# Kernel optimization log

Measured on AMD Instinct MI355X. Metric: run time of the kernel, lower is better.

The kernel has to match this reference:

```python
import jax, jax.numpy as jnp
import numpy as np

B, T, D = 4, 8160, 1024
N, H = 8, 128            # heads, units_per_head (D == N*H)
W = 12                   # block_size
LEFT_CTX = 13            # atten_left_context
L = LEFT_CTX - 1         # left context frames beyond current position
R = 0                    # atten_right_context
C = W + L + R            # context_size = 24
CAP = 50.0               # attention_logits_soft_capping


def _timing_signal(pos, channels):
    # sinusoidal embedding, channels even (1024)
    pos = pos.astype(jnp.float32)
    nt = channels // 2
    inc = np.log(10000.0) / max(nt - 1, 1)
    inv = jnp.exp(jnp.arange(nt, dtype=jnp.float32) * -inc)
    st = pos[:, :, None] * inv[None, None, :]
    return jnp.concatenate([jnp.sin(st), jnp.cos(st)], axis=2)


def _extract_block_context(x, block_size, left, right, pad_val):
    # x: [B, T, ...] -> [B, num_blocks, context_size, ...]
    pads = [(0, 0)] * x.ndim
    pads[1] = (left, right + block_size - 1)
    xp = jnp.pad(x, pads, constant_values=jnp.asarray(pad_val, x.dtype))
    frame_len = block_size + left + right
    num_frames = (xp.shape[1] - frame_len) // block_size + 1
    idx = jnp.arange(num_frames)[:, None] * block_size + jnp.arange(frame_len)[None, :]
    return jnp.take(xp, idx, axis=1)


def _convert_to_block(x, block_size):
    b, t = x.shape[0], x.shape[1]
    nb = t // block_size  # T chosen as multiple of block_size
    return x.reshape((b, nb, block_size) + x.shape[2:])


def setup_inputs() -> dict:
    key = jax.random.key(0)
    ks = jax.random.split(key, 6)
    x = jax.random.normal(ks[0], (B, T, D), dtype=jnp.float32)
    mask = jnp.ones((B, T), dtype=bool)
    i = jnp.arange(W)[:, None]
    j = jnp.arange(C)[None, :]
    causal_valid_mask = (j >= i) & (j - i <= L + R)  # [W, C]
    s = 1.0 / np.sqrt(D)
    wq = jax.random.normal(ks[1], (D, D), dtype=jnp.float32) * s
    wk = jax.random.normal(ks[2], (D, D), dtype=jnp.float32) * s
    wv = jax.random.normal(ks[3], (D, D), dtype=jnp.float32) * s
    pos_proj = jax.random.normal(ks[4], (D, N, H), dtype=jnp.float32) * s
    return {"x": x, "mask": mask, "causal_valid_mask": causal_valid_mask,
            "wq": wq, "wk": wk, "wv": wv, "pos_proj": pos_proj}


def reference(x, mask, causal_valid_mask, wq, wk, wv, pos_proj):
    b, t, d = x.shape
    u = t // W
    q = jnp.einsum('btd,df->btf', x, wq).reshape(b, t, N, H)
    k = jnp.einsum('btd,df->btf', x, wk).reshape(b, t, N, H)
    v = jnp.einsum('btd,df->btf', x, wv).reshape(b, t, N, H)

    q_blk = _convert_to_block(q, W) * (H ** -0.5)        # [B,U,W,N,H]
    k_ctx = _extract_block_context(k, W, L, R, 0.0)      # [B,U,C,N,H]
    v_ctx = _extract_block_context(v, W, L, R, 0.0)      # [B,U,C,N,H]

    # term A+C: content logits
    term_ac = jnp.einsum('BuwNH,BucNH->BNuwc', q_blk, k_ctx)

    # term B+D: relative position logits via skew trick
    pos = jnp.arange(L, -R - 1, -1)[None, :]             # [1, L+R+1]
    sin_emb = _timing_signal(pos, D)                     # [1, L+R+1, D]
    sin_emb = jnp.einsum('fd,dnh->fnh', sin_emb[0], pos_proj)  # [F,N,H]
    term_bd = jnp.einsum('BuwNH,FNH->BNuwF', q_blk, sin_emb)   # [B,N,U,W,F]
    term_bd = jnp.pad(term_bd, ((0, 0),) * 4 + ((0, C + 1 - (L + R + 1)),))
    term_bd = term_bd.reshape(b, N, u, W * (C + 1))[:, :, :, :W * C]
    term_bd = term_bd.reshape(b, N, u, W, C)

    logits = term_ac + term_bd
    logits = CAP * jnp.tanh(logits / CAP)

    mask_ctx = _extract_block_context(mask, W, L, R, False)    # [B,U,C]
    valid = mask_ctx[:, None, :, None, :] & causal_valid_mask[None, None, None, :, :]
    logits = jnp.where(valid, logits, jnp.asarray(-1e9, logits.dtype))
    probs = jax.nn.softmax(logits, axis=-1)              # [B,N,U,W,C]

    out = jnp.einsum('BNuwc,BucNH->BuwNH', probs, v_ctx)
    return out.reshape(b, u * W, N, H)[:, :t]            # [B,T,N,H]
```

## Files before the change

### kernel.cpp

```cpp
#include <hip/hip_runtime.h>
#include <cstdint>
#include <cstddef>


typedef __bf16 bf16_t;
typedef float  floatx4 __attribute__((ext_vector_type(4)));
typedef __bf16 bf16x8  __attribute__((ext_vector_type(8)));
typedef __bf16 bf16x4  __attribute__((ext_vector_type(4)));

#define GLDS16(gp, lp)                                                        \
  __builtin_amdgcn_global_load_lds(                                           \
      (const __attribute__((address_space(1))) void*)(gp),                    \
      (__attribute__((address_space(3))) void*)(lp), 16, 0, 0)

static constexpr int kT     = 8160;
static constexpr int kM     = 4 * kT;
static constexpr int kU     = kT / 12;
static constexpr int kNC    = 3200;

__global__ __launch_bounds__(256) void convert_x(const float* __restrict__ X,
                                                 bf16_t* __restrict__ Xb) {
  const size_t i = ((size_t)blockIdx.x * 256 + threadIdx.x) * 8;
  float4 a = *(const float4*)(X + i);
  float4 b = *(const float4*)(X + i + 4);
  bf16x8 o;
  o[0] = (bf16_t)a.x; o[1] = (bf16_t)a.y; o[2] = (bf16_t)a.z; o[3] = (bf16_t)a.w;
  o[4] = (bf16_t)b.x; o[5] = (bf16_t)b.y; o[6] = (bf16_t)b.z; o[7] = (bf16_t)b.w;
  *(bf16x8*)(Xb + i) = o;
}

__global__ __launch_bounds__(512) void posemb_k(const float* __restrict__ pp,
                                                float* __restrict__ pe) {
  __shared__ float st[1024];
  __shared__ float red[4][128];
  const int d   = blockIdx.x;
  const int fc  = blockIdx.y;
  const int tid = threadIdx.x;
  const float dpos = (float)d;
  for (int i = tid; i < 1024; i += 512) {
    int idx = i & 511;
    float freq = expf(-(float)idx * (9.2103403719761836f / 511.0f));
    float a = dpos * freq;
    st[i] = (i < 512) ? sinf(a) : cosf(a);
  }
  __syncthreads();
  const int part = tid >> 7;
  const int fl   = tid & 127;
  const int f    = fc * 128 + fl;
  float acc = 0.f;
  const int dd0 = part * 256;
  for (int dd = dd0; dd < dd0 + 256; ++dd)
    acc += st[dd] * pp[(size_t)dd * 1024 + f];
  red[part][fl] = acc;
  __syncthreads();
  if (tid < 128)
    pe[(size_t)d * 1024 + f] = red[0][fl] + red[1][fl] + red[2][fl] + red[3][fl];
}

__global__ __launch_bounds__(256) void transpose_w(const float* __restrict__ Wq,
                                                   const float* __restrict__ Wk,
                                                   const float* __restrict__ Wv,
                                                   bf16_t* __restrict__ Wt) {
  __shared__ float tile[64][65];
  const int g = blockIdx.z;
  const float* W = (g == 0) ? Wq : (g == 1) ? Wk : Wv;
  bf16_t* O = Wt + (size_t)g * 1024 * 1024;
  const int k0 = blockIdx.x * 64, n0 = blockIdx.y * 64;
  const int col = threadIdx.x & 63, r4 = threadIdx.x >> 6;
#pragma unroll
  for (int i = 0; i < 16; ++i) {
    int row = i * 4 + r4;
    tile[row][col] = W[(size_t)(k0 + row) * 1024 + n0 + col];
  }
  __syncthreads();
#pragma unroll
  for (int i = 0; i < 16; ++i) {
    int row = i * 4 + r4;
    O[(size_t)(n0 + row) * 1024 + k0 + col] = (bf16_t)tile[col][row];
  }
}

__global__ __launch_bounds__(256) void pe2w(const float* __restrict__ pe,
                                            bf16_t* __restrict__ Wt) {
  const int idx = blockIdx.x;
  const int tid = threadIdx.x;
  bf16_t* out = Wt + (size_t)(3072 + idx) * 1024;
  if (idx >= 104) {
    bf16x4 z = {};
    *(bf16x4*)(out + tid * 4) = z;
    return;
  }
  const int n = idx / 13, d = idx - n * 13;
  __shared__ float peh[128];
  if (tid < 128) peh[tid] = pe[(size_t)d * 1024 + n * 128 + tid];
  __syncthreads();
  float acc[4] = {};
  const bf16_t* wb = Wt + (size_t)(n * 128) * 1024 + tid * 4;
  for (int h = 0; h < 128; ++h) {
    bf16x4 w4 = *(const bf16x4*)(wb + (size_t)h * 1024);
    float s = peh[h];
    acc[0] += s * (float)w4[0];
    acc[1] += s * (float)w4[1];
    acc[2] += s * (float)w4[2];
    acc[3] += s * (float)w4[3];
  }
  bf16x4 o;
  o[0] = (bf16_t)acc[0]; o[1] = (bf16_t)acc[1];
  o[2] = (bf16_t)acc[2]; o[3] = (bf16_t)acc[3];
  *(bf16x4*)(out + tid * 4) = o;
}

__global__ __launch_bounds__(256) void qkv_gemm(const bf16_t* __restrict__ X,
                                                const bf16_t* __restrict__ Wt,
                                                bf16_t* __restrict__ QKV) {
  const int flat = blockIdx.x;
  const int xcd  = flat & 7;
  const int j    = flat >> 3;
  const int work = xcd * 800 + j;
  if (work >= 255 * 25) return;
  const int m0 = (work / 25) * 128;
  const int n0 = (work % 25) * 128;

  __shared__ bf16_t As[128 * 32];
  __shared__ bf16_t Bs[128 * 32];
  const int tid  = threadIdx.x;
  const int wave = tid >> 6;
  const int lane = tid & 63;
  const int wm   = (wave >> 1) * 64;
  const int wn   = (wave & 1) * 64;
  const int qd   = lane >> 4;
  const int lr   = lane & 15;

  floatx4 acc[4][4] = {};

  const int c0 = (wave * 2 + 0) * 64 + lane;
  const int c1 = (wave * 2 + 1) * 64 + lane;
  const int r0 = c0 >> 2, o0 = (c0 & 3) * 8;
  const int r1 = c1 >> 2, o1 = (c1 & 3) * 8;
  const bf16_t* xg0 = X + (size_t)(m0 + r0) * 1024 + o0;
  const bf16_t* xg1 = X + (size_t)(m0 + r1) * 1024 + o1;
  const bf16_t* wg0 = Wt + (size_t)(n0 + r0) * 1024 + o0;
  const bf16_t* wg1 = Wt + (size_t)(n0 + r1) * 1024 + o1;
  bf16_t* lA0 = As + (wave * 2 + 0) * 512;
  bf16_t* lA1 = As + (wave * 2 + 1) * 512;
  bf16_t* lB0 = Bs + (wave * 2 + 0) * 512;
  bf16_t* lB1 = Bs + (wave * 2 + 1) * 512;

  for (int kk = 0; kk < 1024; kk += 32) {
    GLDS16(xg0 + kk, lA0);
    GLDS16(xg1 + kk, lA1);
    GLDS16(wg0 + kk, lB0);
    GLDS16(wg1 + kk, lB1);
    __syncthreads();

    bf16x8 a[4], b[4];
#pragma unroll
    for (int im = 0; im < 4; ++im)
      a[im] = *(const bf16x8*)(As + (wm + im * 16 + lr) * 32 + qd * 8);
#pragma unroll
    for (int in = 0; in < 4; ++in)
      b[in] = *(const bf16x8*)(Bs + (wn + in * 16 + lr) * 32 + qd * 8);
#pragma unroll
    for (int im = 0; im < 4; ++im)
#pragma unroll
      for (int in = 0; in < 4; ++in)
        acc[im][in] = __builtin_amdgcn_mfma_f32_16x16x32_bf16(
            a[im], b[in], acc[im][in], 0, 0, 0);
    __syncthreads();
  }

#pragma unroll
  for (int im = 0; im < 4; ++im)
#pragma unroll
    for (int in = 0; in < 4; ++in)
#pragma unroll
      for (int r = 0; r < 4; ++r) {
        int m = m0 + wm + im * 16 + qd * 4 + r;
        int n = n0 + wn + in * 16 + lr;
        QKV[(size_t)m * kNC + n] = (bf16_t)acc[im][in][r];
      }
}

__global__ __launch_bounds__(256) void attn_k(const bf16_t* __restrict__ QKV,
                                              float* __restrict__ OUT) {
  __shared__ bf16_t qs[12 * 136];
  __shared__ bf16_t ks[24 * 136];
  __shared__ float  vs[24 * 132];
  __shared__ float  qpes[156];
  __shared__ float  p[12 * 16];

  const int flat = blockIdx.x;
  const int xcd  = flat & 7;
  const int jj   = flat >> 3;
  const int u    = xcd * 85 + (jj % 85);
  const int rest = jj / 85;
  const int n    = rest & 7;
  const int b    = rest >> 3;
  const int tid  = threadIdx.x;
  const int t0   = u * 12 - 12;
  const size_t bbase = (size_t)b * kT;

  if (tid < 192) {
    int row = tid >> 4, ch = tid & 15;
    bf16x8 q8 = *(const bf16x8*)(QKV + (bbase + u * 12 + row) * kNC + n * 128 + ch * 8);
    *(bf16x8*)(qs + row * 136 + ch * 8) = q8;
  }
  for (int i = tid; i < 24 * 16; i += 256) {
    int row = i >> 4, ch = i & 15;
    int t = t0 + row;
    int ko = row * 136 + ch * 8;
    int vo = row * 132 + ch * 8;
    if (t < 0) {
      bf16x8 z = {};
      *(bf16x8*)(ks + ko) = z;
      float4 z4 = {};
      *(float4*)(vs + vo) = z4; *(float4*)(vs + vo + 4) = z4;
    } else {
      size_t base = (bbase + t) * kNC + n * 128 + ch * 8;
      bf16x8 k8 = *(const bf16x8*)(QKV + base + 1024);
      bf16x8 v8 = *(const bf16x8*)(QKV + base + 2048);
      *(bf16x8*)(ks + ko) = k8;
      float4 vl = { (float)v8[0], (float)v8[1], (float)v8[2], (float)v8[3] };
      float4 vh = { (float)v8[4], (float)v8[5], (float)v8[6], (float)v8[7] };
      *(float4*)(vs + vo) = vl; *(float4*)(vs + vo + 4) = vh;
    }
  }
  if (tid < 156) {
    int w = tid / 13, d = tid - w * 13;
    qpes[tid] = (float)QKV[(bbase + u * 12 + w) * kNC + 3072 + n * 13 + d];
  }
  __syncthreads();

  if (tid < 156) {
    int w = tid / 13, d = tid - w * 13;
    int t = u * 12 + w - d;
    float lg = -1e30f;
    if (t >= 0) {
      int cc = w - d + 12;
      const bf16_t* qp = qs + w * 136;
      const bf16_t* kp = ks + cc * 136;
      float acc = qpes[tid];
#pragma unroll
      for (int it = 0; it < 16; ++it) {
        bf16x8 q8 = *(const bf16x8*)(qp + it * 8);
        bf16x8 k8 = *(const bf16x8*)(kp + it * 8);
#pragma unroll
        for (int jx = 0; jx < 8; ++jx) acc += (float)q8[jx] * (float)k8[jx];
      }
      lg = 50.0f * tanhf(acc * 0.0017677669529663689f);
    }
    p[w * 16 + d] = lg;
  }
  __syncthreads();

  if (tid < 12) {
    float* pr = p + tid * 16;
    float mx = -1e30f;
#pragma unroll
    for (int d = 0; d < 13; ++d) mx = fmaxf(mx, pr[d]);
    float sum = 0.f;
    float e[13];
#pragma unroll
    for (int d = 0; d < 13; ++d) { e[d] = expf(pr[d] - mx); sum += e[d]; }
    float inv = 1.0f / sum;
#pragma unroll
    for (int d = 0; d < 13; ++d) pr[d] = e[d] * inv;
  }
  __syncthreads();

  for (int i = tid; i < 12 * 32; i += 256) {
    int w = i >> 5, c4 = i & 31;
    const float* pw = p + w * 16;
    float4 acc = {};
#pragma unroll
    for (int d = 0; d < 13; ++d) {
      float pd = pw[d];
      float4 v4 = *(const float4*)(vs + (w - d + 12) * 132 + c4 * 4);
      acc.x += pd * v4.x; acc.y += pd * v4.y;
      acc.z += pd * v4.z; acc.w += pd * v4.w;
    }
    *(float4*)(OUT + (bbase + u * 12 + w) * 1024 + n * 128 + c4 * 4) = acc;
  }
}

extern "C" void kernel_launch(void* const* d_in, const int* in_sizes, int n_in,
                              void* d_out, int out_size, void* d_ws, size_t ws_size,
                              hipStream_t stream) {
  const float* x  = (const float*)d_in[0];
  const float* wq = (const float*)d_in[3];
  const float* wk = (const float*)d_in[4];
  const float* wv = (const float*)d_in[5];
  const float* pp = (const float*)d_in[6];

  char* ws = (char*)d_ws;
  float*  pe  = (float*)ws;
  bf16_t* Wt  = (bf16_t*)(ws + (1u << 16));
  bf16_t* Xb  = (bf16_t*)(ws + (1u << 16) + 8u * 1024 * 1024);
  bf16_t* QKV = (bf16_t*)(ws + (1u << 16) + 8u * 1024 * 1024 +
                          (size_t)kM * 1024 * 2);
  float* out = (float*)d_out;

  convert_x<<<kM * 1024 / (256 * 8), 256, 0, stream>>>(x, Xb);
  posemb_k<<<dim3(13, 8), 512, 0, stream>>>(pp, pe);
  transpose_w<<<dim3(16, 16, 3), 256, 0, stream>>>(wq, wk, wv, Wt);
  pe2w<<<128, 256, 0, stream>>>(pe, Wt);
  qkv_gemm<<<6400, 256, 0, stream>>>(Xb, Wt, QKV);
  attn_k<<<21760, 256, 0, stream>>>(QKV, out);
}
```

Before: 625.7 us.

## Rewrite QKV GEMM with 256x256 tiles, double-buffered LDS and swizzle

```diff
diff --git a/kernel.cpp b/kernel.cpp
--- a/kernel.cpp
+++ b/kernel.cpp
@@ -110,75 +110,146 @@
   *(bf16x4*)(out + tid * 4) = o;
 }
 
-__global__ __launch_bounds__(256) void qkv_gemm(const bf16_t* __restrict__ X,
-                                                const bf16_t* __restrict__ Wt,
-                                                bf16_t* __restrict__ QKV) {
+__global__ __launch_bounds__(512, 2) void qkv_gemm(const bf16_t* __restrict__ X,
+                                                   const bf16_t* __restrict__ Wt,
+                                                   bf16_t* __restrict__ QKV) {
+  __shared__ __align__(16) bf16_t lds[8][8192];
+
   const int flat = blockIdx.x;
-  const int xcd  = flat & 7;
-  const int j    = flat >> 3;
-  const int work = xcd * 800 + j;
-  if (work >= 255 * 25) return;
-  const int m0 = (work / 25) * 128;
-  const int n0 = (work % 25) * 128;
-
-  __shared__ bf16_t As[128 * 32];
-  __shared__ bf16_t Bs[128 * 32];
+  const int work = (flat & 7) * 208 + (flat >> 3);
+  const int mt = work / 13, nt = work % 13;
+  const int m0 = mt * 256, n0 = nt * 256;
+
   const int tid  = threadIdx.x;
   const int wave = tid >> 6;
   const int lane = tid & 63;
-  const int wm   = (wave >> 1) * 64;
-  const int wn   = (wave & 1) * 64;
+  const int wm   = wave >> 2;
+  const int wn   = wave & 3;
   const int qd   = lane >> 4;
   const int lr   = lane & 15;
 
-  floatx4 acc[4][4] = {};
-
-  const int c0 = (wave * 2 + 0) * 64 + lane;
-  const int c1 = (wave * 2 + 1) * 64 + lane;
-  const int r0 = c0 >> 2, o0 = (c0 & 3) * 8;
-  const int r1 = c1 >> 2, o1 = (c1 & 3) * 8;
-  const bf16_t* xg0 = X + (size_t)(m0 + r0) * 1024 + o0;
-  const bf16_t* xg1 = X + (size_t)(m0 + r1) * 1024 + o1;
-  const bf16_t* wg0 = Wt + (size_t)(n0 + r0) * 1024 + o0;
-  const bf16_t* wg1 = Wt + (size_t)(n0 + r1) * 1024 + o1;
-  bf16_t* lA0 = As + (wave * 2 + 0) * 512;
-  bf16_t* lA1 = As + (wave * 2 + 1) * 512;
-  bf16_t* lB0 = Bs + (wave * 2 + 0) * 512;
-  bf16_t* lB1 = Bs + (wave * 2 + 1) * 512;
-
-  for (int kk = 0; kk < 1024; kk += 32) {
-    GLDS16(xg0 + kk, lA0);
-    GLDS16(xg1 + kk, lA1);
-    GLDS16(wg0 + kk, lB0);
-    GLDS16(wg1 + kk, lB1);
-    __syncthreads();
-
-    bf16x8 a[4], b[4];
-#pragma unroll
-    for (int im = 0; im < 4; ++im)
-      a[im] = *(const bf16x8*)(As + (wm + im * 16 + lr) * 32 + qd * 8);
-#pragma unroll
-    for (int in = 0; in < 4; ++in)
-      b[in] = *(const bf16x8*)(Bs + (wn + in * 16 + lr) * 32 + qd * 8);
-#pragma unroll
-    for (int im = 0; im < 4; ++im)
+  const int rr  = tid >> 3;
+  const int cg8 = ((tid & 7) ^ (rr & 7)) * 8;
+  const bf16_t* aP[4];
+  const bf16_t* bP[4];
+  {
+    int r2 = m0 + 128 + rr, r3 = m0 + 192 + rr;
+    aP[0] = X + (size_t)(m0 + rr) * 1024 + cg8;
+    aP[1] = X + (size_t)(m0 + 64 + rr) * 1024 + cg8;
+    aP[2] = X + (size_t)(r2 < kM ? r2 : 0) * 1024 + cg8;
+    aP[3] = X + (size_t)(r3 < kM ? r3 : 0) * 1024 + cg8;
+    int s2 = n0 + 128 + rr, s3 = n0 + 192 + rr;
+    bP[0] = Wt + (size_t)(n0 + rr) * 1024 + cg8;
+    bP[1] = Wt + (size_t)(n0 + 64 + rr) * 1024 + cg8;
+    bP[2] = Wt + (size_t)(s2 < kNC ? s2 : 0) * 1024 + cg8;
+    bP[3] = Wt + (size_t)(s3 < kNC ? s3 : 0) * 1024 + cg8;
+  }
+
+#define STAGE_A(h, t)                                                          \
+  do {                                                                         \
+    bf16_t* d_ = &lds[((t) & 1) * 4 + (h)][wave * 512];                        \
+    GLDS16(aP[2 * (h)]     + (size_t)(t) * 64, d_);                            \
+    GLDS16(aP[2 * (h) + 1] + (size_t)(t) * 64, d_ + 4096);                     \
+  } while (0)
+#define STAGE_B(h, t)                                                          \
+  do {                                                                         \
+    bf16_t* d_ = &lds[((t) & 1) * 4 + 2 + (h)][wave * 512];                    \
+    GLDS16(bP[2 * (h)]     + (size_t)(t) * 64, d_);                            \
+    GLDS16(bP[2 * (h) + 1] + (size_t)(t) * 64, d_ + 4096);                     \
+  } while (0)
+
+  auto frag = [&](int slot, int r, int cb) -> bf16x8 {
+    uint32_t off = (uint32_t)(r * 128 + cb) ^ (uint32_t)((r & 7) << 4);
+    return *(const bf16x8*)((const char*)&lds[slot][0] + off);
+  };
+
+  floatx4 acc[8][4] = {};
+
+  STAGE_A(0, 0); STAGE_A(1, 0); STAGE_B(0, 0); STAGE_B(1, 0);
+  STAGE_B(0, 1); STAGE_B(1, 1);
+  asm volatile("s_waitcnt vmcnt(4)" ::: "memory");
+  __builtin_amdgcn_s_barrier();
+
+  const int aslot0 = wm;
+  const int bslot0 = 2 + (wn >> 1);
+  const int brow0  = (wn & 1) * 64;
+
+#pragma unroll 2
+  for (int t = 0; t < 16; ++t) {
+    const int par = (t & 1) * 4;
+    bf16x8 bfrag[4][2];
+#pragma unroll
+    for (int p = 0; p < 4; ++p) {
+      if (p == 0) {
+#pragma unroll
+        for (int in = 0; in < 4; ++in)
+#pragma unroll
+          for (int k2 = 0; k2 < 2; ++k2)
+            bfrag[in][k2] =
+                frag(par + bslot0, brow0 + in * 16 + lr, k2 * 64 + qd * 16);
+      }
+      bf16x8 afrag[2][2];
+#pragma unroll
+      for (int i = 0; i < 2; ++i)
+#pragma unroll
+        for (int k2 = 0; k2 < 2; ++k2)
+          afrag[i][k2] =
+              frag(par + aslot0, (2 * p + i) * 16 + lr, k2 * 64 + qd * 16);
+
+      if (p == 0)      { if (t < 15) STAGE_A(0, t + 1); }
+      else if (p == 1) { if (t < 15) STAGE_A(1, t + 1); }
+      else if (p == 2) { if (t < 14) STAGE_B(0, t + 2); }
+      else             { if (t < 14) STAGE_B(1, t + 2); }
+
+      if (p == 3) {
+        if (t < 14) asm volatile("s_waitcnt vmcnt(4)" ::: "memory");
+        else        asm volatile("s_waitcnt vmcnt(0)" ::: "memory");
+      }
+      __builtin_amdgcn_s_barrier();
+      asm volatile("s_waitcnt lgkmcnt(0)" ::: "memory");
+      __builtin_amdgcn_sched_barrier(0);
+
+      __builtin_amdgcn_s_setprio(1);
+#pragma unroll
+      for (int i = 0; i < 2; ++i)
+#pragma unroll
+        for (int in = 0; in < 4; ++in)
+#pragma unroll
+          for (int k2 = 0; k2 < 2; ++k2)
+            acc[2 * p + i][in] = __builtin_amdgcn_mfma_f32_16x16x32_bf16(
+                afrag[i][k2], bfrag[in][k2], acc[2 * p + i][in], 0, 0, 0);
+      __builtin_amdgcn_s_setprio(0);
+      __builtin_amdgcn_sched_barrier(0);
+      __builtin_amdgcn_s_barrier();
+    }
+  }
+#undef STAGE_A
+#undef STAGE_B
+
+  const int mBase = m0 + wm * 128 + qd * 4;
+  const int nBase = n0 + wn * 64 + lr;
+  if (m0 + 256 <= kM && n0 + 256 <= kNC) {
+#pragma unroll
+    for (int im = 0; im < 8; ++im)
 #pragma unroll
       for (int in = 0; in < 4; ++in)
-        acc[im][in] = __builtin_amdgcn_mfma_f32_16x16x32_bf16(
-            a[im], b[in], acc[im][in], 0, 0, 0);
-    __syncthreads();
-  }
-
-#pragma unroll
-  for (int im = 0; im < 4; ++im)
-#pragma unroll
-    for (int in = 0; in < 4; ++in)
-#pragma unroll
-      for (int r = 0; r < 4; ++r) {
-        int m = m0 + wm + im * 16 + qd * 4 + r;
-        int n = n0 + wn + in * 16 + lr;
-        QKV[(size_t)m * kNC + n] = (bf16_t)acc[im][in][r];
-      }
+#pragma unroll
+        for (int r = 0; r < 4; ++r)
+          QKV[(size_t)(mBase + im * 16 + r) * kNC + nBase + in * 16] =
+              (bf16_t)acc[im][in][r];
+  } else {
+#pragma unroll
+    for (int im = 0; im < 8; ++im)
+#pragma unroll
+      for (int in = 0; in < 4; ++in)
+#pragma unroll
+        for (int r = 0; r < 4; ++r) {
+          int m = mBase + im * 16 + r;
+          int n = nBase + in * 16;
+          if (m < kM && n < kNC)
+            QKV[(size_t)m * kNC + n] = (bf16_t)acc[im][in][r];
+        }
+  }
 }
 
 __global__ __launch_bounds__(256) void attn_k(const bf16_t* __restrict__ QKV,
@@ -304,6 +375,6 @@
   posemb_k<<<dim3(13, 8), 512, 0, stream>>>(pp, pe);
   transpose_w<<<dim3(16, 16, 3), 256, 0, stream>>>(wq, wk, wv, Wt);
   pe2w<<<128, 256, 0, stream>>>(pe, Wt);
-  qkv_gemm<<<6400, 256, 0, stream>>>(Xb, Wt, QKV);
+  qkv_gemm<<<1664, 512, 0, stream>>>(Xb, Wt, QKV);
   attn_k<<<21760, 256, 0, stream>>>(QKV, out);
 }
```

New measurement: 586.3 us. 1.07x faster.
